# Performance work log

Hardware: AMD Instinct MI355X
Metric: run time of the kernel (lower is better)

Reference implementation:

```python
import jax, jax.numpy as jnp
import numpy as np

B, F, H, OUT, S = 32768, 256, 128, 64, 6
RELAX, EPS, BN_EPS = 1.5, 1e-05, 1e-05
SQRT_HALF = 0.7071067811865476


def _bn(h, g, b):
    # training-mode BatchNorm1d: biased batch statistics over dim 0
    m = h.mean(axis=0)
    v = h.var(axis=0)
    return (h - m) * jax.lax.rsqrt(v + BN_EPS) * g + b


def _tfrm(x, W, g, b, glu_act=True):
    h = _bn(x @ W, g, b)
    if glu_act:
        d = h.shape[1] // 2
        h = h[:, :d] * jax.nn.sigmoid(h[:, d:])
    return h


def setup_inputs() -> dict:
    key = jax.random.key(0)
    ks = jax.random.split(key, 6)
    f32 = jnp.float32
    return {
        "x": jax.random.normal(ks[0], (B, F), f32),
        "enc_g": jnp.ones((F,), f32), "enc_b": jnp.zeros((F,), f32),
        "W1": jax.random.normal(ks[1], (F, 2 * H), f32) * 0.05,
        "g1": jnp.ones((2 * H,), f32), "b1": jnp.zeros((2 * H,), f32),
        "W2": jax.random.normal(ks[2], (H, 2 * H), f32) * 0.05,
        "g2": jnp.ones((2 * H,), f32), "b2": jnp.zeros((2 * H,), f32),
        "W3": jax.random.normal(ks[3], (S, H, 2 * H), f32) * 0.05,
        "g3": jnp.ones((S, 2 * H), f32), "b3": jnp.zeros((S, 2 * H), f32),
        "W4": jax.random.normal(ks[4], (S, H, 2 * H), f32) * 0.05,
        "g4": jnp.ones((S, 2 * H), f32), "b4": jnp.zeros((S, 2 * H), f32),
        "Wc": jax.random.normal(ks[5], (S - 1, OUT, F), f32) * 0.05,
        "gc": jnp.ones((S - 1, F), f32), "bc": jnp.zeros((S - 1, F), f32),
    }


def reference(x, enc_g, enc_b, W1, g1, b1, W2, g2, b2, W3, g3, b3,
              W4, g4, b4, Wc, gc, bc):
    x = _bn(x, enc_g, enc_b)                      # [B, F]
    masked = x
    compl = jnp.ones((x.shape[0], F), x.dtype)    # complementary aggregated mask
    agg_out, agg_entropy = [], []
    for ni in range(S):
        h = _tfrm(masked, W1, g1, b1)                             # [B, H]
        h = (_tfrm(h, W2, g2, b2) + h) * SQRT_HALF
        h = (_tfrm(h, W3[ni], g3[ni], b3[ni]) + h) * SQRT_HALF
        h = (_tfrm(h, W4[ni], g4[ni], b4[ni]) + h) * SQRT_HALF
        if ni > 0:
            # NOTE: source uses x (not h) here -- replicated faithfully
            agg_out.append(jax.nn.relu(x[:, :OUT]))
        fc = h[:, OUT:]                                           # [B, OUT]
        if ni < S - 1:
            coef = _tfrm(fc, Wc[ni], gc[ni], bc[ni], glu_act=False)  # [B, F]
            mask_values = jax.nn.softmax(coef * compl, axis=1)
            compl = compl * (RELAX - mask_values)
            agg_entropy.append(
                jnp.mean(jnp.sum(-mask_values * jnp.log(mask_values + EPS), axis=1))
                / (S - 1))
            masked = mask_values * x
    out = jnp.sum(jnp.stack(agg_out, axis=0), axis=0)   # [B, OUT]
    entropy = jnp.sum(jnp.stack(agg_entropy))           # scalar
    return (out, entropy)
```

## Files before the change

### kernel.cpp

```cpp
#include <hip/hip_runtime.h>
#include <math.h>

#define BSZ   32768
#define FDIM  256
#define HDIM  128
#define OUTD  64
#define SQRT_HALF 0.70710678118654752f
#define BN_EPS 1e-5f
#define SM_EPS 1e-5f
#define INV_B (1.0f / 32768.0f)
#define NCPY  8
#define SLOT  (NCPY * 512)
#define GRID  1024

#define SWZ(r, cb) ((((r) << 9) + (cb)) ^ (((r) & 7) << 4))

typedef __attribute__((ext_vector_type(8))) short bf16x8;
typedef __attribute__((ext_vector_type(4))) short bf16x4;
typedef __attribute__((ext_vector_type(4))) float f32x4;

__device__ __forceinline__ float b2f(unsigned short u) {
    return __uint_as_float(((unsigned int)u) << 16);
}
__device__ __forceinline__ unsigned short f2b(float f) {
    unsigned int u = __float_as_uint(f);
    u += 0x7fff + ((u >> 16) & 1);
    return (unsigned short)(u >> 16);
}

__device__ __forceinline__ void async16(const void* g, void* l) {
    __builtin_amdgcn_global_load_lds(
        (const __attribute__((address_space(1))) void*)(uintptr_t)g,
        (__attribute__((address_space(3))) void*)(unsigned int)(uintptr_t)l,
        16, 0, 0);
}

__device__ inline float waveMaxAll(float v) {
#pragma unroll
    for (int m = 32; m > 0; m >>= 1) v = fmaxf(v, __shfl_xor(v, m, 64));
    return v;
}
__device__ inline float waveSumAll(float v) {
#pragma unroll
    for (int m = 32; m > 0; m >>= 1) v += __shfl_xor(v, m, 64);
    return v;
}

__device__ __forceinline__ void grid_sync_sw(unsigned int* bar, unsigned int nb) {
    __syncthreads();
    if (threadIdx.x == 0) {
        __threadfence();
        unsigned int gen = __hip_atomic_load(bar + 1, __ATOMIC_RELAXED, __HIP_MEMORY_SCOPE_AGENT);
        unsigned int arr = __hip_atomic_fetch_add(bar, 1u, __ATOMIC_ACQ_REL, __HIP_MEMORY_SCOPE_AGENT);
        if (arr == nb - 1) {
            __hip_atomic_store(bar, 0u, __ATOMIC_RELAXED, __HIP_MEMORY_SCOPE_AGENT);
            __hip_atomic_fetch_add(bar + 1, 1u, __ATOMIC_RELEASE, __HIP_MEMORY_SCOPE_AGENT);
        } else {
            long spin = 0;
            while (__hip_atomic_load(bar + 1, __ATOMIC_ACQUIRE, __HIP_MEMORY_SCOPE_AGENT) == gen) {
                if (++spin > (1L << 24)) break;
                __builtin_amdgcn_s_sleep(2);
            }
        }
        __threadfence();
    }
    __syncthreads();
}

__device__ __forceinline__ void stage_B(short* Bs, const unsigned short* __restrict__ Wt,
                                        int K, int k0, int wave, int lane) {
    const int sr = lane >> 2;
    const int sc = (lane & 3) * 8;
#pragma unroll
    for (int t = 0; t < 4; ++t) {
        const int wr = wave * 64 + t * 16 + sr;
        async16(Wt + (size_t)wr * K + k0 + sc, (void*)(Bs + (wave * 4 + t) * 512 + lane * 8));
    }
}

__device__ __forceinline__ void gemm_core(const short* buf, short* Bs,
                                          const unsigned short* __restrict__ Wt, int K,
                                          int wave, int lane, f32x4 (&acc)[2][4]) {
    const int fm = lane & 15;
    const int fq = (lane >> 4) * 8;
#pragma unroll
    for (int i = 0; i < 2; ++i)
#pragma unroll
        for (int j = 0; j < 4; ++j)
            acc[i][j] = (f32x4){0.f, 0.f, 0.f, 0.f};

    for (int k0 = 0; k0 < K; k0 += 32) {
        __syncthreads();
        bf16x8 af[2], bfr[4];
#pragma unroll
        for (int i = 0; i < 2; ++i)
            af[i] = *(const bf16x8*)((const char*)buf + SWZ(i * 16 + fm, (k0 + fq) * 2));
#pragma unroll
        for (int j = 0; j < 4; ++j)
            bfr[j] = *(const bf16x8*)(Bs + (wave * 64 + j * 16 + fm) * 32 + fq);
#pragma unroll
        for (int i = 0; i < 2; ++i)
#pragma unroll
            for (int j = 0; j < 4; ++j)
                acc[i][j] = __builtin_amdgcn_mfma_f32_16x16x32_bf16(af[i], bfr[j], acc[i][j], 0, 0, 0);
        __syncthreads();
        if (k0 + 32 < K) stage_B(Bs, Wt, K, k0 + 32, wave, lane);
    }
}

__device__ __forceinline__ void stage_epilogue(f32x4 (&acc)[2][4], short* buf,
                                               float* redS, float* redQ,
                                               float* __restrict__ statsOut,
                                               int wave, int lane, int tid, int bcp) {
    const int fm = lane & 15;
    const int row4 = (lane >> 4) * 4;
    const int ocol = wave * 64 + fm;
#pragma unroll
    for (int i = 0; i < 2; ++i)
#pragma unroll
        for (int j = 0; j < 4; ++j)
#pragma unroll
            for (int r = 0; r < 4; ++r)
                *(short*)((char*)buf + SWZ(row4 + i * 16 + r, (ocol + j * 16) * 2)) =
                    (short)f2b(acc[i][j][r]);

#pragma unroll
    for (int j = 0; j < 4; ++j) {
        float s = 0.f, q = 0.f;
#pragma unroll
        for (int i = 0; i < 2; ++i)
#pragma unroll
            for (int r = 0; r < 4; ++r) {
                float v = acc[i][j][r];
                s += v; q += v * v;
            }
        s += __shfl_xor(s, 16, 64); s += __shfl_xor(s, 32, 64);
        q += __shfl_xor(q, 16, 64); q += __shfl_xor(q, 32, 64);
        if (lane < 16) {
            redS[wave * 64 + j * 16 + lane] = s;
            redQ[wave * 64 + j * 16 + lane] = q;
        }
    }
    __syncthreads();
    atomicAdd(&statsOut[bcp + tid], redS[tid]);
    atomicAdd(&statsOut[bcp + 256 + tid], redQ[tid]);
}

__device__ __forceinline__ void build_tbl_glu(const float* __restrict__ st,
                                              const float* __restrict__ pg,
                                              const float* __restrict__ pb,
                                              int colOff, int K, int tid, float* tbl) {
    if (tid < K) {
        const int ch = colOff + tid;
        const int cg = ch + 128;
        float sA = 0.f, qA = 0.f, sG = 0.f, qG = 0.f;
#pragma unroll
        for (int cp = 0; cp < NCPY; ++cp) {
            const float* p = st + cp * 512;
            sA += p[ch]; qA += p[256 + ch];
            sG += p[cg]; qG += p[256 + cg];
        }
        float ma = sA * INV_B, va = qA * INV_B - ma * ma;
        float scA = pg[ch] * rsqrtf(va + BN_EPS);
        tbl[tid] = scA; tbl[K + tid] = pb[ch] - ma * scA;
        float mg = sG * INV_B, vg = qG * INV_B - mg * mg;
        float scG = pg[cg] * rsqrtf(vg + BN_EPS);
        tbl[2 * K + tid] = scG; tbl[3 * K + tid] = pb[cg] - mg * scG;
    }
    __syncthreads();
}

__device__ __forceinline__ void build_tbl_mask(const float* __restrict__ st,
                                               const float* __restrict__ gcp,
                                               const float* __restrict__ bcp_,
                                               int tid, float* tbl) {
    float s = 0.f, q = 0.f;
#pragma unroll
    for (int cp = 0; cp < NCPY; ++cp) {
        s += st[cp * 512 + tid];
        q += st[cp * 512 + 256 + tid];
    }
    float mean = s * INV_B, var = q * INV_B - mean * mean;
    float scl = gcp[tid] * rsqrtf(var + BN_EPS);
    tbl[tid] = scl;
    tbl[256 + tid] = bcp_[tid] - mean * scl;
    __syncthreads();
}

template <int K, bool RES, bool WH, int RB>
__device__ __forceinline__ void glu_prologue(short* buf, const float* tbl,
                                             int tid, int colOff, bf16x4* h) {
    const int ar = tid >> 3;
    const int ac = (tid & 7) * 4;
#pragma unroll
    for (int c = 0; c < K / 32; ++c) {
        const int kk = c * 32 + ac;
        bf16x4 lo = *(const bf16x4*)((const char*)buf + SWZ(ar, (colOff + kk) * 2));
        bf16x4 hi = *(const bf16x4*)((const char*)buf + SWZ(ar, (colOff + kk + 128) * 2));
        float4 a0 = *(const float4*)&tbl[kk];
        float4 h0 = *(const float4*)&tbl[K + kk];
        float4 g0 = *(const float4*)&tbl[2 * K + kk];
        float4 s0 = *(const float4*)&tbl[3 * K + kk];
        const float scA[4] = {a0.x, a0.y, a0.z, a0.w};
        const float shA[4] = {h0.x, h0.y, h0.z, h0.w};
        const float scG[4] = {g0.x, g0.y, g0.z, g0.w};
        const float shG[4] = {s0.x, s0.y, s0.z, s0.w};
        bf16x4 o4;
#pragma unroll
        for (int e = 0; e < 4; ++e) {
            float na = b2f((unsigned short)lo[e]) * scA[e] + shA[e];
            float ng = b2f((unsigned short)hi[e]) * scG[e] + shG[e];
            float v = na * (1.0f / (1.0f + __expf(-ng)));
            if (RES) v = (v + b2f((unsigned short)h[RB + c][e])) * SQRT_HALF;
            o4[e] = (short)f2b(v);
        }
        *(bf16x4*)((char*)buf + SWZ(ar, kk * 2)) = o4;
        if (WH) h[c] = o4;
    }
}

template <int MODE>
__device__ __forceinline__ void mask_phase(short* buf, const float* tbl,
                                           const unsigned short* __restrict__ xb,
                                           unsigned short* cmpl, float* ent, float* went,
                                           int tid, int wave, int lane, int row0, int bid) {
    const int r = tid >> 3;
    const int cq = tid & 7;
    const size_t grow = (size_t)(row0 + r) * 256;

    float l[32];
    float mx = -1e30f;
#pragma unroll
    for (int e = 0; e < 4; ++e) {
        const int c = cq * 32 + e * 8;
        bf16x8 pv = *(const bf16x8*)((const char*)buf + SWZ(r, c * 2));
        bf16x8 cv;
        if (MODE != 0) cv = *(const bf16x8*)(cmpl + grow + c);
        float4 s0 = *(const float4*)&tbl[c], s1 = *(const float4*)&tbl[c + 4];
        float4 h0 = *(const float4*)&tbl[256 + c], h1 = *(const float4*)&tbl[256 + c + 4];
        const float* sp0 = (const float*)&s0; const float* sp1 = (const float*)&s1;
        const float* hp0 = (const float*)&h0; const float* hp1 = (const float*)&h1;
#pragma unroll
        for (int t = 0; t < 8; ++t) {
            float scl = (t < 4) ? sp0[t] : sp1[t - 4];
            float shf = (t < 4) ? hp0[t] : hp1[t - 4];
            float cl = (MODE != 0) ? b2f((unsigned short)cv[t]) : 1.0f;
            float v = (b2f((unsigned short)pv[t]) * scl + shf) * cl;
            l[e * 8 + t] = v;
            mx = fmaxf(mx, v);
        }
    }
    mx = fmaxf(mx, __shfl_xor(mx, 1, 64));
    mx = fmaxf(mx, __shfl_xor(mx, 2, 64));
    mx = fmaxf(mx, __shfl_xor(mx, 4, 64));

    float ssum = 0.f;
#pragma unroll
    for (int i = 0; i < 32; ++i) { l[i] = __expf(l[i] - mx); ssum += l[i]; }
    ssum += __shfl_xor(ssum, 1, 64);
    ssum += __shfl_xor(ssum, 2, 64);
    ssum += __shfl_xor(ssum, 4, 64);
    const float inv = 1.0f / ssum;

    float et = 0.f;
#pragma unroll
    for (int e = 0; e < 4; ++e) {
        const int c = cq * 32 + e * 8;
        bf16x8 xv, cv2;
        if (MODE != 2) xv = *(const bf16x8*)(xb + grow + c);
        if (MODE == 1) cv2 = *(const bf16x8*)(cmpl + grow + c);
        bf16x8 mo, co;
#pragma unroll
        for (int t = 0; t < 8; ++t) {
            float m = l[e * 8 + t] * inv;
            et -= m * __logf(m + SM_EPS);
            if (MODE != 2) {
                float cl = (MODE == 1) ? b2f((unsigned short)cv2[t]) : 1.0f;
                co[t] = (short)f2b(cl * (1.5f - m));
                mo[t] = (short)f2b(m * b2f((unsigned short)xv[t]));
            }
        }
        if (MODE != 2) {
            *(bf16x8*)(cmpl + grow + c) = co;
            *(bf16x8*)((char*)buf + SWZ(r, c * 2)) = mo;
        }
    }
    et += __shfl_xor(et, 1, 64);
    et += __shfl_xor(et, 2, 64);
    et += __shfl_xor(et, 4, 64);
    float wet = waveSumAll(et) * 0.125f;
    if (lane == 0) went[wave] = wet;
    __syncthreads();
    if (tid == 0) {
        float v = went[0] + went[1] + went[2] + went[3];
        atomicAdd(&ent[(bid & 255) << 5], v * (INV_B * 0.2f));
    }
}

__global__ __launch_bounds__(256, 4) void mega(
    const float* __restrict__ x,
    const float* __restrict__ enc_g, const float* __restrict__ enc_b,
    const float* __restrict__ g1, const float* __restrict__ b1,
    const float* __restrict__ g2, const float* __restrict__ b2,
    const float* __restrict__ g3, const float* __restrict__ b3,
    const float* __restrict__ g4, const float* __restrict__ b4,
    const float* __restrict__ gc, const float* __restrict__ bc,
    const float* __restrict__ W1f, const float* __restrict__ W2f,
    const float* __restrict__ W3f, const float* __restrict__ W4f,
    const float* __restrict__ Wcf,
    unsigned short* __restrict__ W1t, unsigned short* __restrict__ W2t,
    unsigned short* __restrict__ W3t, unsigned short* __restrict__ W4t,
    unsigned short* __restrict__ Wct,
    unsigned short* __restrict__ xb, unsigned short* __restrict__ cmpl,
    float* __restrict__ stats, float* __restrict__ ent,
    unsigned int* __restrict__ bar,
    float* __restrict__ out)
{
#define GSYNC() grid_sync_sw(bar, GRID)

    __shared__ short buf[32 * 256];
    __shared__ short Bs[256 * 32];
    __shared__ float redS[256], redQ[256];
    __shared__ float tbl[512];
    __shared__ float went[4];

    const int tid  = threadIdx.x;
    const int wave = tid >> 6;
    const int lane = tid & 63;
    const int bid  = blockIdx.x;
    const int row0 = bid * 32;
    const int bcp  = (bid & (NCPY - 1)) * 512;

    if (bid < 136) {
        const int m = bid >> 3, kz = bid & 7, n = tid;
        const float* src; unsigned short* dst; int K;
        if (m == 0)      { src = W1f;                        dst = W1t;               K = 256; }
        else if (m == 1) { src = W2f;                        dst = W2t;               K = 128; }
        else if (m < 7)  { int i = m - 2;  src = W3f + (size_t)i * 128 * 256; dst = W3t + (size_t)i * 32768; K = 128; }
        else if (m < 12) { int i = m - 7;  src = W4f + (size_t)i * 128 * 256; dst = W4t + (size_t)i * 32768; K = 128; }
        else             { int i = m - 12; src = Wcf + (size_t)i * 64 * 256;  dst = Wct + (size_t)i * 16384; K = 64; }
        const int k0 = kz * 32;
        if (k0 < K)
            for (int k = k0; k < k0 + 32; ++k)
                dst[(size_t)n * K + k] = f2b(src[(size_t)k * 256 + n]);
    }
    {
        float* red = (float*)buf;
        const int sub = wave;
        const int c4  = lane << 2;
        float s[4] = {0.f, 0.f, 0.f, 0.f}, q[4] = {0.f, 0.f, 0.f, 0.f};
#pragma unroll 8
        for (int i = 0; i < 8; ++i) {
            const int row = row0 + i * 4 + sub;
            float4 v = *(const float4*)(x + (size_t)row * 256 + c4);
            s[0] += v.x; q[0] += v.x * v.x;
            s[1] += v.y; q[1] += v.y * v.y;
            s[2] += v.z; q[2] += v.z * v.z;
            s[3] += v.w; q[3] += v.w * v.w;
        }
#pragma unroll
        for (int e = 0; e < 4; ++e) {
            red[sub * 512 + c4 + e] = s[e];
            red[sub * 512 + 256 + c4 + e] = q[e];
        }
        __syncthreads();
        float sS = red[tid] + red[512 + tid] + red[1024 + tid] + red[1536 + tid];
        float sQ = red[256 + tid] + red[768 + tid] + red[1280 + tid] + red[1792 + tid];
        atomicAdd(&stats[bcp + tid], sS);
        atomicAdd(&stats[bcp + 256 + tid], sQ);
    }
    GSYNC();

    stage_B(Bs, W1t, 256, 0, wave, lane);
    {
        float s = 0.f, q = 0.f;
#pragma unroll
        for (int cp = 0; cp < NCPY; ++cp) {
            s += stats[cp * 512 + tid];
            q += stats[cp * 512 + 256 + tid];
        }
        float mean = s * INV_B, var = q * INV_B - mean * mean;
        float scl = enc_g[tid] * rsqrtf(var + BN_EPS);
        tbl[tid] = scl;
        tbl[256 + tid] = enc_b[tid] - mean * scl;
    }
    __syncthreads();
    {
        const int r = tid >> 3, cq = tid & 7;
        const size_t grow = (size_t)(row0 + r) * 256;
#pragma unroll
        for (int e = 0; e < 4; ++e) {
            const int c = cq * 32 + e * 8;
            float4 xa = *(const float4*)(x + grow + c);
            float4 xc = *(const float4*)(x + grow + c + 4);
            const float xv[8] = {xa.x, xa.y, xa.z, xa.w, xc.x, xc.y, xc.z, xc.w};
            float4 s0 = *(const float4*)&tbl[c], s1 = *(const float4*)&tbl[c + 4];
            float4 f0 = *(const float4*)&tbl[256 + c], f1 = *(const float4*)&tbl[256 + c + 4];
            const float sc[8] = {s0.x, s0.y, s0.z, s0.w, s1.x, s1.y, s1.z, s1.w};
            const float sh[8] = {f0.x, f0.y, f0.z, f0.w, f1.x, f1.y, f1.z, f1.w};
            float n[8];
            bf16x8 o8;
#pragma unroll
            for (int t = 0; t < 8; ++t) {
                n[t] = xv[t] * sc[t] + sh[t];
                o8[t] = (short)f2b(n[t]);
            }
            *(bf16x8*)((char*)buf + SWZ(r, c * 2)) = o8;
            *(bf16x8*)(xb + grow + c) = o8;
            if (c < OUTD) {
                float4 o1 = make_float4(5.f * fmaxf(n[0], 0.f), 5.f * fmaxf(n[1], 0.f),
                                        5.f * fmaxf(n[2], 0.f), 5.f * fmaxf(n[3], 0.f));
                float4 o2 = make_float4(5.f * fmaxf(n[4], 0.f), 5.f * fmaxf(n[5], 0.f),
                                        5.f * fmaxf(n[6], 0.f), 5.f * fmaxf(n[7], 0.f));
                *(float4*)(out + (size_t)(row0 + r) * OUTD + c) = o1;
                *(float4*)(out + (size_t)(row0 + r) * OUTD + c + 4) = o2;
            }
        }
    }

    f32x4 acc[2][4];
    bf16x4 h[4];

    for (int ni = 0; ni < 5; ++ni) {
        float* s1 = stats + (size_t)(1 + ni * 5 + 0) * SLOT;
        float* s2 = stats + (size_t)(1 + ni * 5 + 1) * SLOT;
        float* s3 = stats + (size_t)(1 + ni * 5 + 2) * SLOT;
        float* s4 = stats + (size_t)(1 + ni * 5 + 3) * SLOT;
        float* s5 = stats + (size_t)(1 + ni * 5 + 4) * SLOT;

        if (ni > 0) {
            stage_B(Bs, W1t, 256, 0, wave, lane);
            float* s5p = stats + (size_t)(1 + (ni - 1) * 5 + 4) * SLOT;
            build_tbl_mask(s5p, gc + (ni - 1) * 256, bc + (ni - 1) * 256, tid, tbl);
            if (ni == 1)
                mask_phase<0>(buf, tbl, xb, cmpl, ent, went, tid, wave, lane, row0, bid);
            else
                mask_phase<1>(buf, tbl, xb, cmpl, ent, went, tid, wave, lane, row0, bid);
        }
        gemm_core(buf, Bs, W1t, 256, wave, lane, acc);
        stage_epilogue(acc, buf, redS, redQ, s1, wave, lane, tid, bcp);
        GSYNC();

        stage_B(Bs, W2t, 128, 0, wave, lane);
        build_tbl_glu(s1, g1, b1, 0, 128, tid, tbl);
        glu_prologue<128, false, true, 0>(buf, tbl, tid, 0, h);
        gemm_core(buf, Bs, W2t, 128, wave, lane, acc);
        stage_epilogue(acc, buf, redS, redQ, s2, wave, lane, tid, bcp);
        GSYNC();

        {
            const unsigned short* Wt = W3t + (size_t)ni * 32768;
            stage_B(Bs, Wt, 128, 0, wave, lane);
            build_tbl_glu(s2, g2, b2, 0, 128, tid, tbl);
            glu_prologue<128, true, true, 0>(buf, tbl, tid, 0, h);
            gemm_core(buf, Bs, Wt, 128, wave, lane, acc);
            stage_epilogue(acc, buf, redS, redQ, s3, wave, lane, tid, bcp);
        }
        GSYNC();

        {
            const unsigned short* Wt = W4t + (size_t)ni * 32768;
            stage_B(Bs, Wt, 128, 0, wave, lane);
            build_tbl_glu(s3, g3 + ni * 256, b3 + ni * 256, 0, 128, tid, tbl);
            glu_prologue<128, true, true, 0>(buf, tbl, tid, 0, h);
            gemm_core(buf, Bs, Wt, 128, wave, lane, acc);
            stage_epilogue(acc, buf, redS, redQ, s4, wave, lane, tid, bcp);
        }
        GSYNC();

        {
            const unsigned short* Wt = Wct + (size_t)ni * 16384;
            stage_B(Bs, Wt, 64, 0, wave, lane);
            build_tbl_glu(s4, g4 + ni * 256, b4 + ni * 256, 64, 64, tid, tbl);
            glu_prologue<64, true, false, 2>(buf, tbl, tid, 64, h);
            gemm_core(buf, Bs, Wt, 64, wave, lane, acc);
            stage_epilogue(acc, buf, redS, redQ, s5, wave, lane, tid, bcp);
        }
        GSYNC();
    }

    build_tbl_mask(stats + (size_t)(1 + 4 * 5 + 4) * SLOT,
                   gc + 4 * 256, bc + 4 * 256, tid, tbl);
    mask_phase<2>(buf, tbl, xb, cmpl, ent, went, tid, wave, lane, row0, bid);
    GSYNC();

    if (bid == 0 && wave == 0) {
        float v = 0.f;
#pragma unroll
        for (int i = 0; i < 4; ++i) v += ent[(lane + 64 * i) << 5];
        v = waveSumAll(v);
        if (lane == 0) out[(size_t)BSZ * OUTD] = v;
    }
#undef GSYNC
}

__global__ __launch_bounds__(256) void prep_w(
    const float* __restrict__ W1, const float* __restrict__ W2,
    const float* __restrict__ W3, const float* __restrict__ W4,
    const float* __restrict__ Wc,
    unsigned short* __restrict__ W1t, unsigned short* __restrict__ W2t,
    unsigned short* __restrict__ W3t, unsigned short* __restrict__ W4t,
    unsigned short* __restrict__ Wct)
{
    const int m = blockIdx.x, kz = blockIdx.y, n = threadIdx.x;
    const float* src; unsigned short* dst; int K;
    if (m == 0)      { src = W1;                        dst = W1t;               K = 256; }
    else if (m == 1) { src = W2;                        dst = W2t;               K = 128; }
    else if (m < 7)  { int i = m - 2;  src = W3 + (size_t)i * 128 * 256; dst = W3t + (size_t)i * 32768; K = 128; }
    else if (m < 12) { int i = m - 7;  src = W4 + (size_t)i * 128 * 256; dst = W4t + (size_t)i * 32768; K = 128; }
    else             { int i = m - 12; src = Wc + (size_t)i * 64 * 256;  dst = Wct + (size_t)i * 16384; K = 64; }
    const int k0 = kz * 32;
    if (k0 >= K) return;
    for (int k = k0; k < k0 + 32; ++k)
        dst[(size_t)n * K + k] = f2b(src[(size_t)k * 256 + n]);
}

__global__ __launch_bounds__(256) void colstats(const float* __restrict__ X,
                                                float* __restrict__ st0) {
    __shared__ float red[4][512];
    const int sub = threadIdx.x >> 6;
    const int c4  = (threadIdx.x & 63) << 2;
    float s[4] = {0.f, 0.f, 0.f, 0.f}, q[4] = {0.f, 0.f, 0.f, 0.f};
#pragma unroll 8
    for (int i = 0; i < 8; ++i) {
        const int row = blockIdx.x * 32 + i * 4 + sub;
        float4 v = *(const float4*)(X + (size_t)row * 256 + c4);
        s[0] += v.x; q[0] += v.x * v.x;
        s[1] += v.y; q[1] += v.y * v.y;
        s[2] += v.z; q[2] += v.z * v.z;
        s[3] += v.w; q[3] += v.w * v.w;
    }
#pragma unroll
    for (int e = 0; e < 4; ++e) {
        red[sub][c4 + e] = s[e];
        red[sub][256 + c4 + e] = q[e];
    }
    __syncthreads();
    const int t = threadIdx.x;
    const int cp = (blockIdx.x & (NCPY - 1)) * 512;
    float sS = red[0][t] + red[1][t] + red[2][t] + red[3][t];
    float sQ = red[0][256 + t] + red[1][256 + t] + red[2][256 + t] + red[3][256 + t];
    atomicAdd(&st0[cp + t], sS);
    atomicAdd(&st0[cp + 256 + t], sQ);
}

__global__ __launch_bounds__(256) void norm_x(const float* __restrict__ x,
                                              const float* __restrict__ st0,
                                              const float* __restrict__ g,
                                              const float* __restrict__ b,
                                              unsigned short* __restrict__ xb,
                                              float* __restrict__ out) {
    const int i4 = blockIdx.x * 256 + threadIdx.x;
    const int row = i4 >> 6, c4 = (i4 & 63) << 2;
    float4 xv = *(const float4*)(x + (size_t)row * 256 + c4);
    float sS[4] = {0.f, 0.f, 0.f, 0.f}, sQ[4] = {0.f, 0.f, 0.f, 0.f};
#pragma unroll
    for (int cp = 0; cp < NCPY; ++cp) {
        float4 a = *(const float4*)&st0[cp * 512 + c4];
        float4 q = *(const float4*)&st0[cp * 512 + 256 + c4];
        sS[0] += a.x; sS[1] += a.y; sS[2] += a.z; sS[3] += a.w;
        sQ[0] += q.x; sQ[1] += q.y; sQ[2] += q.z; sQ[3] += q.w;
    }
    float4 gv = *(const float4*)&g[c4];
    float4 bv = *(const float4*)&b[c4];
    const float* xp = (const float*)&xv;
    const float* gp = (const float*)&gv; const float* bp = (const float*)&bv;
    float n[4];
    ushort4 ob;
    unsigned short* obp = (unsigned short*)&ob;
#pragma unroll
    for (int e = 0; e < 4; ++e) {
        float mean = sS[e] * INV_B;
        float var  = sQ[e] * INV_B - mean * mean;
        float sc   = gp[e] * rsqrtf(var + BN_EPS);
        float sh   = bp[e] - mean * sc;
        n[e] = xp[e] * sc + sh;
        obp[e] = f2b(n[e]);
    }
    *(ushort4*)(xb + (size_t)row * 256 + c4) = ob;
    if (c4 < OUTD) {
        float4 ov = make_float4(5.0f * fmaxf(n[0], 0.f), 5.0f * fmaxf(n[1], 0.f),
                                5.0f * fmaxf(n[2], 0.f), 5.0f * fmaxf(n[3], 0.f));
        *(float4*)(out + (size_t)row * OUTD + c4) = ov;
    }
}

__device__ __forceinline__ void gemm_epilogue(
    f32x4 (&acc)[2][4], int row0, int wave, int lane, int tid, int bcp,
    float* redS, float* redQ,
    unsigned short* __restrict__ Pout, float* __restrict__ statsOut)
{
    const int fm = lane & 15;
    const int orow = row0 + (lane >> 4) * 4;
    const int ocol = wave * 64 + fm;
#pragma unroll
    for (int i = 0; i < 2; ++i)
#pragma unroll
        for (int j = 0; j < 4; ++j)
#pragma unroll
            for (int r = 0; r < 4; ++r)
                Pout[(size_t)(orow + i * 16 + r) * 256 + (ocol + j * 16)] = f2b(acc[i][j][r]);

#pragma unroll
    for (int j = 0; j < 4; ++j) {
        float s = 0.f, q = 0.f;
#pragma unroll
        for (int i = 0; i < 2; ++i)
#pragma unroll
            for (int r = 0; r < 4; ++r) {
                float v = acc[i][j][r];
                s += v; q += v * v;
            }
        s += __shfl_xor(s, 16, 64); s += __shfl_xor(s, 32, 64);
        q += __shfl_xor(q, 16, 64); q += __shfl_xor(q, 32, 64);
        if (lane < 16) {
            redS[wave * 64 + j * 16 + lane] = s;
            redQ[wave * 64 + j * 16 + lane] = q;
        }
    }
    __syncthreads();
    atomicAdd(&statsOut[bcp + tid], redS[tid]);
    atomicAdd(&statsOut[bcp + 256 + tid], redQ[tid]);
}

__global__ __launch_bounds__(256) void gemm_bf16(
    const unsigned short* __restrict__ A,
    const unsigned short* __restrict__ Wt, int K,
    unsigned short* __restrict__ P,
    float* __restrict__ statsOut)
{
    __shared__ short As[32 * 32];
    __shared__ short Bs[256 * 32];
    __shared__ float redS[256], redQ[256];

    const int tid  = threadIdx.x;
    const int wave = tid >> 6;
    const int lane = tid & 63;
    const int row0 = blockIdx.x * 32;
    const int bcp  = (blockIdx.x & (NCPY - 1)) * 512;

    const int sr = lane >> 2;
    const int sc = (lane & 3) * 8;
    const int fm = lane & 15;
    const int fq = (lane >> 4) * 8;

    f32x4 acc[2][4];
#pragma unroll
    for (int i = 0; i < 2; ++i)
#pragma unroll
        for (int j = 0; j < 4; ++j)
            acc[i][j] = (f32x4){0.f, 0.f, 0.f, 0.f};

    for (int k0 = 0; k0 < K; k0 += 32) {
        if (wave < 2)
            async16(A + (size_t)(row0 + wave * 16 + sr) * K + k0 + sc,
                    (void*)(As + wave * 512 + lane * 8));
#pragma unroll
        for (int t = 0; t < 4; ++t) {
            const int wr = wave * 64 + t * 16 + sr;
            async16(Wt + (size_t)wr * K + k0 + sc,
                    (void*)(Bs + (wave * 4 + t) * 512 + lane * 8));
        }
        __syncthreads();

        bf16x8 af[2], bfr[4];
#pragma unroll
        for (int i = 0; i < 2; ++i)
            af[i] = *(const bf16x8*)(As + (i * 16 + fm) * 32 + fq);
#pragma unroll
        for (int j = 0; j < 4; ++j)
            bfr[j] = *(const bf16x8*)(Bs + (wave * 64 + j * 16 + fm) * 32 + fq);
#pragma unroll
        for (int i = 0; i < 2; ++i)
#pragma unroll
            for (int j = 0; j < 4; ++j)
                acc[i][j] = __builtin_amdgcn_mfma_f32_16x16x32_bf16(af[i], bfr[j], acc[i][j], 0, 0, 0);
        __syncthreads();
    }

    gemm_epilogue(acc, row0, wave, lane, tid, bcp, redS, redQ, P, statsOut);
}

template <int MODE>
__global__ __launch_bounds__(256) void gemm_mask(
    const unsigned short* Pc,
    const float* __restrict__ cstats,
    const float* __restrict__ gc, const float* __restrict__ bc,
    const unsigned short* __restrict__ xb,
    unsigned short* __restrict__ cmpl,
    float* __restrict__ ent,
    const unsigned short* __restrict__ Wt,
    unsigned short* Pout,
    float* __restrict__ statsOut)
{
    __shared__ short Am[32 * 256];
    __shared__ short Bs[256 * 32];
    __shared__ float redS[256], redQ[256];
    __shared__ float tScl[256], tShf[256];
    __shared__ float went[4];

    const int tid  = threadIdx.x;
    const int wave = tid >> 6;
    const int lane = tid & 63;
    const int row0 = blockIdx.x * 32;
    const int bcp  = (blockIdx.x & (NCPY - 1)) * 512;

    const int sr = lane >> 2;
    const int sc = (lane & 3) * 8;

#pragma unroll
    for (int t = 0; t < 4; ++t) {
        const int wr = wave * 64 + t * 16 + sr;
        async16(Wt + (size_t)wr * 256 + sc,
                (void*)(Bs + (wave * 4 + t) * 512 + lane * 8));
    }

    {
        float s = 0.f, q = 0.f;
#pragma unroll
        for (int cp = 0; cp < NCPY; ++cp) {
            s += cstats[cp * 512 + tid];
            q += cstats[cp * 512 + 256 + tid];
        }
        float mean = s * INV_B, var = q * INV_B - mean * mean;
        float scl_ = gc[tid] * rsqrtf(var + BN_EPS);
        tScl[tid] = scl_;
        tShf[tid] = bc[tid] - mean * scl_;
    }
    __syncthreads();

    const int r  = tid >> 3;
    const int cq = tid & 7;
    const size_t grow = (size_t)(row0 + r) * 256;

    float l[32];
    float mx = -1e30f;
#pragma unroll
    for (int e = 0; e < 4; ++e) {
        const int c = cq * 32 + e * 8;
        bf16x8 pv = *(const bf16x8*)(Pc + grow + c);
        bf16x8 cv;
        if (MODE) cv = *(const bf16x8*)(cmpl + grow + c);
        float4 s0 = *(const float4*)&tScl[c], s1 = *(const float4*)&tScl[c + 4];
        float4 h0 = *(const float4*)&tShf[c], h1 = *(const float4*)&tShf[c + 4];
        const float* sp0 = (const float*)&s0; const float* sp1 = (const float*)&s1;
        const float* hp0 = (const float*)&h0; const float* hp1 = (const float*)&h1;
#pragma unroll
        for (int t = 0; t < 8; ++t) {
            float scl_ = (t < 4) ? sp0[t] : sp1[t - 4];
            float shf_ = (t < 4) ? hp0[t] : hp1[t - 4];
            float cl = MODE ? b2f((unsigned short)cv[t]) : 1.0f;
            float v = (b2f((unsigned short)pv[t]) * scl_ + shf_) * cl;
            l[e * 8 + t] = v;
            mx = fmaxf(mx, v);
        }
    }
    mx = fmaxf(mx, __shfl_xor(mx, 1, 64));
    mx = fmaxf(mx, __shfl_xor(mx, 2, 64));
    mx = fmaxf(mx, __shfl_xor(mx, 4, 64));

    float ssum = 0.f;
#pragma unroll
    for (int i = 0; i < 32; ++i) { l[i] = __expf(l[i] - mx); ssum += l[i]; }
    ssum += __shfl_xor(ssum, 1, 64);
    ssum += __shfl_xor(ssum, 2, 64);
    ssum += __shfl_xor(ssum, 4, 64);
    const float inv = 1.0f / ssum;

    float et = 0.f;
#pragma unroll
    for (int e = 0; e < 4; ++e) {
        const int c = cq * 32 + e * 8;
        bf16x8 xv = *(const bf16x8*)(xb + grow + c);
        bf16x8 cv2;
        if (MODE) cv2 = *(const bf16x8*)(cmpl + grow + c);
        bf16x8 mo, co;
#pragma unroll
        for (int t = 0; t < 8; ++t) {
            float m = l[e * 8 + t] * inv;
            et -= m * __logf(m + SM_EPS);
            float cl = MODE ? b2f((unsigned short)cv2[t]) : 1.0f;
            co[t] = (short)f2b(cl * (1.5f - m));
            mo[t] = (short)f2b(m * b2f((unsigned short)xv[t]));
        }
        *(bf16x8*)(cmpl + grow + c) = co;
        unsigned int byte = (unsigned int)(r * 512 + c * 2);
        byte ^= ((unsigned int)(r & 7)) << 4;
        *(bf16x8*)((char*)Am + byte) = mo;
    }
    et += __shfl_xor(et, 1, 64);
    et += __shfl_xor(et, 2, 64);
    et += __shfl_xor(et, 4, 64);
    float wet = waveSumAll(et) * 0.125f;
    if (lane == 0) went[wave] = wet;
    __syncthreads();
    if (tid == 0) {
        float v = went[0] + went[1] + went[2] + went[3];
        atomicAdd(&ent[(blockIdx.x & 255) << 5], v * (INV_B * 0.2f));
    }

    const int fm = lane & 15;
    const int fq = (lane >> 4) * 8;

    f32x4 acc[2][4];
#pragma unroll
    for (int i = 0; i < 2; ++i)
#pragma unroll
        for (int j = 0; j < 4; ++j)
            acc[i][j] = (f32x4){0.f, 0.f, 0.f, 0.f};

    for (int k0 = 0; k0 < 256; k0 += 32) {
        bf16x8 af[2], bfr[4];
#pragma unroll
        for (int i = 0; i < 2; ++i) {
            const int row = i * 16 + fm;
            unsigned int byte = (unsigned int)(row * 512 + (k0 + fq) * 2);
            byte ^= ((unsigned int)(row & 7)) << 4;
            af[i] = *(const bf16x8*)((const char*)Am + byte);
        }
#pragma unroll
        for (int j = 0; j < 4; ++j)
            bfr[j] = *(const bf16x8*)(Bs + (wave * 64 + j * 16 + fm) * 32 + fq);
#pragma unroll
        for (int i = 0; i < 2; ++i)
#pragma unroll
            for (int j = 0; j < 4; ++j)
                acc[i][j] = __builtin_amdgcn_mfma_f32_16x16x32_bf16(af[i], bfr[j], acc[i][j], 0, 0, 0);
        __syncthreads();
        if (k0 + 32 < 256) {
#pragma unroll
            for (int t = 0; t < 4; ++t) {
                const int wr = wave * 64 + t * 16 + sr;
                async16(Wt + (size_t)wr * 256 + (k0 + 32) + sc,
                        (void*)(Bs + (wave * 4 + t) * 512 + lane * 8));
            }
            __syncthreads();
        }
    }

    gemm_epilogue(acc, row0, wave, lane, tid, bcp, redS, redQ, Pout, statsOut);
}

template <bool RES, bool WRITE_H>
__global__ __launch_bounds__(256) void gemm_glu(
    const unsigned short* __restrict__ Pprev,
    const float* __restrict__ pstats,
    const float* __restrict__ pg,
    const float* __restrict__ pb,
    const unsigned short* __restrict__ res,
    int colOff,
    const unsigned short* __restrict__ Wt, int K,
    unsigned short* __restrict__ Pout,
    float* __restrict__ statsOut,
    unsigned short* __restrict__ hOut)
{
    __shared__ short As[32 * 32];
    __shared__ short Bs[256 * 32];
    __shared__ float redS[256], redQ[256];
    __shared__ float tScA[128], tShA[128], tScG[128], tShG[128];

    const int tid  = threadIdx.x;
    const int wave = tid >> 6;
    const int lane = tid & 63;
    const int row0 = blockIdx.x * 32;
    const int bcp  = (blockIdx.x & (NCPY - 1)) * 512;

    if (tid < K) {
        const int ch = colOff + tid;
        const int cg = ch + 128;
        float sA = 0.f, qA = 0.f, sG = 0.f, qG = 0.f;
#pragma unroll
        for (int cp = 0; cp < NCPY; ++cp) {
            const float* p = pstats + cp * 512;
            sA += p[ch]; qA += p[256 + ch];
            sG += p[cg]; qG += p[256 + cg];
        }
        float ma = sA * INV_B, va = qA * INV_B - ma * ma;
        float scA = pg[ch] * rsqrtf(va + BN_EPS);
        tScA[tid] = scA; tShA[tid] = pb[ch] - ma * scA;
        float mg = sG * INV_B, vg = qG * INV_B - mg * mg;
        float scG = pg[cg] * rsqrtf(vg + BN_EPS);
        tScG[tid] = scG; tShG[tid] = pb[cg] - mg * scG;
    }
    __syncthreads();

    const int sr = lane >> 2;
    const int sc = (lane & 3) * 8;
    const int ar = tid >> 3;
    const int ac = (tid & 7) * 4;
    const int fm = lane & 15;
    const int fq = (lane >> 4) * 8;

    f32x4 acc[2][4];
#pragma unroll
    for (int i = 0; i < 2; ++i)
#pragma unroll
        for (int j = 0; j < 4; ++j)
            acc[i][j] = (f32x4){0.f, 0.f, 0.f, 0.f};

    for (int k0 = 0; k0 < K; k0 += 32) {
#pragma unroll
        for (int t = 0; t < 4; ++t) {
            const int wr = wave * 64 + t * 16 + sr;
            async16(Wt + (size_t)wr * K + k0 + sc,
                    (void*)(Bs + (wave * 4 + t) * 512 + lane * 8));
        }

        {
            const int kk = k0 + ac;
            const size_t grow = (size_t)(row0 + ar);

            bf16x4 lo = *(const bf16x4*)(Pprev + grow * 256 + colOff + kk);
            bf16x4 hi = *(const bf16x4*)(Pprev + grow * 256 + colOff + kk + 128);
            bf16x4 rv;
            if (RES) rv = *(const bf16x4*)(res + grow * 128 + kk);

            float4 a0 = *(const float4*)&tScA[kk];
            float4 h0 = *(const float4*)&tShA[kk];
            float4 g0 = *(const float4*)&tScG[kk];
            float4 s0 = *(const float4*)&tShG[kk];
            float scA[4] = {a0.x, a0.y, a0.z, a0.w};
            float shA[4] = {h0.x, h0.y, h0.z, h0.w};
            float scG[4] = {g0.x, g0.y, g0.z, g0.w};
            float shG[4] = {s0.x, s0.y, s0.z, s0.w};

            bf16x4 o4;
#pragma unroll
            for (int e = 0; e < 4; ++e) {
                float na = b2f((unsigned short)lo[e]) * scA[e] + shA[e];
                float ng = b2f((unsigned short)hi[e]) * scG[e] + shG[e];
                float v = na * (1.0f / (1.0f + __expf(-ng)));
                if (RES) v = (v + b2f((unsigned short)rv[e])) * SQRT_HALF;
                o4[e] = (short)f2b(v);
            }
            *(bf16x4*)(As + ar * 32 + ac) = o4;
            if (WRITE_H)
                *(bf16x4*)(hOut + grow * 128 + kk) = o4;
        }
        __syncthreads();

        bf16x8 af[2], bfr[4];
#pragma unroll
        for (int i = 0; i < 2; ++i)
            af[i] = *(const bf16x8*)(As + (i * 16 + fm) * 32 + fq);
#pragma unroll
        for (int j = 0; j < 4; ++j)
            bfr[j] = *(const bf16x8*)(Bs + (wave * 64 + j * 16 + fm) * 32 + fq);
#pragma unroll
        for (int i = 0; i < 2; ++i)
#pragma unroll
            for (int j = 0; j < 4; ++j)
                acc[i][j] = __builtin_amdgcn_mfma_f32_16x16x32_bf16(af[i], bfr[j], acc[i][j], 0, 0, 0);
        __syncthreads();
    }

    gemm_epilogue(acc, row0, wave, lane, tid, bcp, redS, redQ, Pout, statsOut);
}

__global__ __launch_bounds__(256) void coef_ent(const unsigned short* __restrict__ Pc,
                                                const float* __restrict__ stats,
                                                const float* __restrict__ gc,
                                                const float* __restrict__ bc,
                                                const unsigned short* __restrict__ cmpl,
                                                float* __restrict__ ent) {
    const int w    = threadIdx.x >> 6;
    const int lane = threadIdx.x & 63;
    const int row  = blockIdx.x * 4 + w;
    const int c    = lane << 2;
    __shared__ float went[4];

    float sS[4] = {0.f, 0.f, 0.f, 0.f}, sQ[4] = {0.f, 0.f, 0.f, 0.f};
#pragma unroll
    for (int cp = 0; cp < NCPY; ++cp) {
        float4 a = *(const float4*)&stats[cp * 512 + c];
        float4 q = *(const float4*)&stats[cp * 512 + 256 + c];
        sS[0] += a.x; sS[1] += a.y; sS[2] += a.z; sS[3] += a.w;
        sQ[0] += q.x; sQ[1] += q.y; sQ[2] += q.z; sQ[3] += q.w;
    }
    float4 gv = *(const float4*)&gc[c];
    float4 bv = *(const float4*)&bc[c];
    const float* gvv = (const float*)&gv; const float* bvv = (const float*)&bv;

    float scl[4], shf[4];
#pragma unroll
    for (int e = 0; e < 4; ++e) {
        float mean = sS[e] * INV_B, var = sQ[e] * INV_B - mean * mean;
        scl[e] = gvv[e] * rsqrtf(var + BN_EPS);
        shf[e] = bvv[e] - mean * scl[e];
    }

    const size_t idx = (size_t)row * 256 + c;
    ushort4 pu = *(const ushort4*)(Pc + idx);
    const unsigned short* puv = (const unsigned short*)&pu;
    ushort4 cu = *(const ushort4*)(cmpl + idx);
    const unsigned short* cuv = (const unsigned short*)&cu;

    float l[4];
#pragma unroll
    for (int e = 0; e < 4; ++e)
        l[e] = (b2f(puv[e]) * scl[e] + shf[e]) * b2f(cuv[e]);

    float mx = waveMaxAll(fmaxf(fmaxf(l[0], l[1]), fmaxf(l[2], l[3])));
    float e0 = __expf(l[0] - mx), e1 = __expf(l[1] - mx),
          e2 = __expf(l[2] - mx), e3 = __expf(l[3] - mx);
    float inv = 1.0f / waveSumAll(e0 + e1 + e2 + e3);

    float m[4] = {e0 * inv, e1 * inv, e2 * inv, e3 * inv};

    float et = -m[0] * __logf(m[0] + SM_EPS) - m[1] * __logf(m[1] + SM_EPS)
             - m[2] * __logf(m[2] + SM_EPS) - m[3] * __logf(m[3] + SM_EPS);
    et = waveSumAll(et);
    if (lane == 0) went[w] = et;
    __syncthreads();
    if (threadIdx.x == 0) {
        float v = went[0] + went[1] + went[2] + went[3];
        atomicAdd(&ent[(blockIdx.x & 255) << 5], v * (INV_B * 0.2f));
    }
}

__global__ __launch_bounds__(64) void write_ent(const float* __restrict__ ent,
                                                float* __restrict__ dst) {
    const int lane = threadIdx.x;
    float v = 0.f;
#pragma unroll
    for (int i = 0; i < 4; ++i) v += ent[(lane + 64 * i) << 5];
    v = waveSumAll(v);
    if (lane == 0) dst[0] = v;
}

extern "C" void kernel_launch(void* const* d_in, const int* in_sizes, int n_in,
                              void* d_out, int out_size, void* d_ws, size_t ws_size,
                              hipStream_t stream) {
    const float* x     = (const float*)d_in[0];
    const float* enc_g = (const float*)d_in[1];
    const float* enc_b = (const float*)d_in[2];
    const float* W1 = (const float*)d_in[3];
    const float* g1 = (const float*)d_in[4];
    const float* b1 = (const float*)d_in[5];
    const float* W2 = (const float*)d_in[6];
    const float* g2 = (const float*)d_in[7];
    const float* b2 = (const float*)d_in[8];
    const float* W3 = (const float*)d_in[9];
    const float* g3 = (const float*)d_in[10];
    const float* b3 = (const float*)d_in[11];
    const float* W4 = (const float*)d_in[12];
    const float* g4 = (const float*)d_in[13];
    const float* b4 = (const float*)d_in[14];
    const float* Wc = (const float*)d_in[15];
    const float* gc = (const float*)d_in[16];
    const float* bc = (const float*)d_in[17];
    float* out = (float*)d_out;

    const size_t NBF = (size_t)BSZ * FDIM;
    const size_t NBH = (size_t)BSZ * HDIM;

    unsigned short* xb     = (unsigned short*)d_ws;
    unsigned short* masked = xb + NBF;
    unsigned short* Pb1    = masked + NBF;
    unsigned short* h1     = Pb1 + NBF;
    unsigned short* h2     = h1 + NBH;
    unsigned short* h3     = h2 + NBH;
    unsigned short* cmpl   = h3 + NBH;
    unsigned short* W1t    = cmpl + NBF;
    unsigned short* W2t    = W1t + 65536;
    unsigned short* W3t    = W2t + 32768;
    unsigned short* W4t    = W3t + 163840;
    unsigned short* Wct    = W4t + 163840;
    float* stats = (float*)(Wct + 81920);
    float* ent   = stats + 26 * SLOT;
    unsigned int* bar = (unsigned int*)masked;

    unsigned short* Pb2 = masked;

    static int s_ok = -1;
    if (s_ok < 0) {
        int occ = 0, mpc = 0, dev = 0;
        hipGetDevice(&dev);
        hipDeviceProp_t prop;
        if (hipGetDeviceProperties(&prop, dev) == hipSuccess) mpc = prop.multiProcessorCount;
        if (hipOccupancyMaxActiveBlocksPerMultiprocessor(
                &occ, reinterpret_cast<const void*>(mega), 256, 0) != hipSuccess) occ = 0;
        s_ok = (occ >= 4 && occ * mpc >= GRID) ? 1 : 0;
    }

    hipMemsetAsync(stats, 0, (26 * SLOT + 256 * 32) * sizeof(float), stream);

    if (s_ok) {
        hipMemsetAsync(bar, 0, 2 * sizeof(unsigned int), stream);
        mega<<<GRID, 256, 0, stream>>>(
            x, enc_g, enc_b, g1, b1, g2, b2, g3, b3, g4, b4, gc, bc,
            W1, W2, W3, W4, Wc, W1t, W2t, W3t, W4t, Wct,
            xb, cmpl, stats, ent, bar, out);
        return;
    }

    prep_w<<<dim3(17, 8), 256, 0, stream>>>(W1, W2, W3, W4, Wc, W1t, W2t, W3t, W4t, Wct);
    colstats<<<1024, 256, 0, stream>>>(x, stats);
    norm_x<<<8192, 256, 0, stream>>>(x, stats, enc_g, enc_b, xb, out);

    for (int ni = 0; ni < 5; ++ni) {
        float* s1 = stats + (size_t)(1 + ni * 5 + 0) * SLOT;
        float* s2 = stats + (size_t)(1 + ni * 5 + 1) * SLOT;
        float* s3 = stats + (size_t)(1 + ni * 5 + 2) * SLOT;
        float* s4 = stats + (size_t)(1 + ni * 5 + 3) * SLOT;
        float* s5 = stats + (size_t)(1 + ni * 5 + 4) * SLOT;

        if (ni == 0) {
            gemm_bf16<<<1024, 256, 0, stream>>>(xb, W1t, 256, Pb1, s1);
        } else {
            float* s5p = stats + (size_t)(1 + (ni - 1) * 5 + 4) * SLOT;
            if (ni == 1)
                gemm_mask<0><<<1024, 256, 0, stream>>>(
                    Pb1, s5p, gc, bc, xb, cmpl, ent, W1t, Pb1, s1);
            else
                gemm_mask<1><<<1024, 256, 0, stream>>>(
                    Pb1, s5p, gc + (ni - 1) * 256, bc + (ni - 1) * 256,
                    xb, cmpl, ent, W1t, Pb1, s1);
        }

        gemm_glu<false, true><<<1024, 256, 0, stream>>>(
            Pb1, s1, g1, b1, nullptr, 0, W2t, 128, Pb2, s2, h1);
        gemm_glu<true, true><<<1024, 256, 0, stream>>>(
            Pb2, s2, g2, b2, h1, 0, W3t + (size_t)ni * 32768, 128, Pb1, s3, h2);
        gemm_glu<true, true><<<1024, 256, 0, stream>>>(
            Pb1, s3, g3 + ni * 256, b3 + ni * 256, h2, 0,
            W4t + (size_t)ni * 32768, 128, Pb2, s4, h3);
        gemm_glu<true, false><<<1024, 256, 0, stream>>>(
            Pb2, s4, g4 + ni * 256, b4 + ni * 256, h3 + 64, 64,
            Wct + (size_t)ni * 16384, 64, Pb1, s5, nullptr);
    }

    coef_ent<<<BSZ / 4, 256, 0, stream>>>(
        Pb1, stats + (size_t)(1 + 4 * 5 + 4) * SLOT,
        gc + 4 * 256, bc + 4 * 256, cmpl, ent);

    write_ent<<<1, 64, 0, stream>>>(ent, out + (size_t)BSZ * OUTD);
}
```

Measured before the change: 565.5 us.

## Replace central grid barrier with striped counters and prefetch next weights before sync

The single-counter generation barrier becomes 64 striped monotonic counters. Each block increments one counter and 64 threads poll all of them against a running target, which spreads atomic contention and removes the reset step. The first weight tile of the next stage is now issued asynchronously before the barrier, so its load overlaps the wait. This relies on the staged B tile not being overwritten by anything in between, and on the barrier memory being enlarged and zeroed each launch.

```diff
diff --git a/kernel.cpp b/kernel.cpp
--- a/kernel.cpp
+++ b/kernel.cpp
@@ -46,21 +46,20 @@
     return v;
 }
 
-__device__ __forceinline__ void grid_sync_sw(unsigned int* bar, unsigned int nb) {
-    __syncthreads();
-    if (threadIdx.x == 0) {
+__device__ __forceinline__ void grid_sync_tree(unsigned int* arr, unsigned int want,
+                                               int bid, int tid) {
+    __syncthreads();
+    if (tid == 0) {
         __threadfence();
-        unsigned int gen = __hip_atomic_load(bar + 1, __ATOMIC_RELAXED, __HIP_MEMORY_SCOPE_AGENT);
-        unsigned int arr = __hip_atomic_fetch_add(bar, 1u, __ATOMIC_ACQ_REL, __HIP_MEMORY_SCOPE_AGENT);
-        if (arr == nb - 1) {
-            __hip_atomic_store(bar, 0u, __ATOMIC_RELAXED, __HIP_MEMORY_SCOPE_AGENT);
-            __hip_atomic_fetch_add(bar + 1, 1u, __ATOMIC_RELEASE, __HIP_MEMORY_SCOPE_AGENT);
-        } else {
-            long spin = 0;
-            while (__hip_atomic_load(bar + 1, __ATOMIC_ACQUIRE, __HIP_MEMORY_SCOPE_AGENT) == gen) {
-                if (++spin > (1L << 24)) break;
-                __builtin_amdgcn_s_sleep(2);
-            }
+        __hip_atomic_fetch_add(&arr[(bid & 63) << 5], 1u,
+                               __ATOMIC_RELEASE, __HIP_MEMORY_SCOPE_AGENT);
+    }
+    if (tid < 64) {
+        unsigned int* p = &arr[tid << 5];
+        long spin = 0;
+        while (__hip_atomic_load(p, __ATOMIC_ACQUIRE, __HIP_MEMORY_SCOPE_AGENT) < want) {
+            if (++spin > (1L << 24)) break;
+            __builtin_amdgcn_s_sleep(1);
         }
         __threadfence();
     }
@@ -316,8 +315,6 @@
     unsigned int* __restrict__ bar,
     float* __restrict__ out)
 {
-#define GSYNC() grid_sync_sw(bar, GRID)
-
     __shared__ short buf[32 * 256];
     __shared__ short Bs[256 * 32];
     __shared__ float redS[256], redQ[256];
@@ -330,6 +327,9 @@
     const int bid  = blockIdx.x;
     const int row0 = bid * 32;
     const int bcp  = (bid & (NCPY - 1)) * 512;
+
+    unsigned int bgen = 0;
+#define GSYNC() do { ++bgen; grid_sync_tree(bar, bgen * 16u, bid, tid); } while (0)
 
     if (bid < 136) {
         const int m = bid >> 3, kz = bid & 7, n = tid;
@@ -429,7 +429,6 @@
         float* s5 = stats + (size_t)(1 + ni * 5 + 4) * SLOT;
 
         if (ni > 0) {
-            stage_B(Bs, W1t, 256, 0, wave, lane);
             float* s5p = stats + (size_t)(1 + (ni - 1) * 5 + 4) * SLOT;
             build_tbl_mask(s5p, gc + (ni - 1) * 256, bc + (ni - 1) * 256, tid, tbl);
             if (ni == 1)
@@ -439,43 +438,35 @@
         }
         gemm_core(buf, Bs, W1t, 256, wave, lane, acc);
         stage_epilogue(acc, buf, redS, redQ, s1, wave, lane, tid, bcp);
+        stage_B(Bs, W2t, 128, 0, wave, lane);
         GSYNC();
 
-        stage_B(Bs, W2t, 128, 0, wave, lane);
         build_tbl_glu(s1, g1, b1, 0, 128, tid, tbl);
         glu_prologue<128, false, true, 0>(buf, tbl, tid, 0, h);
         gemm_core(buf, Bs, W2t, 128, wave, lane, acc);
         stage_epilogue(acc, buf, redS, redQ, s2, wave, lane, tid, bcp);
+        stage_B(Bs, W3t + (size_t)ni * 32768, 128, 0, wave, lane);
         GSYNC();
 
-        {
-            const unsigned short* Wt = W3t + (size_t)ni * 32768;
-            stage_B(Bs, Wt, 128, 0, wave, lane);
-            build_tbl_glu(s2, g2, b2, 0, 128, tid, tbl);
-            glu_prologue<128, true, true, 0>(buf, tbl, tid, 0, h);
-            gemm_core(buf, Bs, Wt, 128, wave, lane, acc);
-            stage_epilogue(acc, buf, redS, redQ, s3, wave, lane, tid, bcp);
-        }
+        build_tbl_glu(s2, g2, b2, 0, 128, tid, tbl);
+        glu_prologue<128, true, true, 0>(buf, tbl, tid, 0, h);
+        gemm_core(buf, Bs, W3t + (size_t)ni * 32768, 128, wave, lane, acc);
+        stage_epilogue(acc, buf, redS, redQ, s3, wave, lane, tid, bcp);
+        stage_B(Bs, W4t + (size_t)ni * 32768, 128, 0, wave, lane);
         GSYNC();
 
-        {
-            const unsigned short* Wt = W4t + (size_t)ni * 32768;
-            stage_B(Bs, Wt, 128, 0, wave, lane);
-            build_tbl_glu(s3, g3 + ni * 256, b3 + ni * 256, 0, 128, tid, tbl);
-            glu_prologue<128, true, true, 0>(buf, tbl, tid, 0, h);
-            gemm_core(buf, Bs, Wt, 128, wave, lane, acc);
-            stage_epilogue(acc, buf, redS, redQ, s4, wave, lane, tid, bcp);
-        }
+        build_tbl_glu(s3, g3 + ni * 256, b3 + ni * 256, 0, 128, tid, tbl);
+        glu_prologue<128, true, true, 0>(buf, tbl, tid, 0, h);
+        gemm_core(buf, Bs, W4t + (size_t)ni * 32768, 128, wave, lane, acc);
+        stage_epilogue(acc, buf, redS, redQ, s4, wave, lane, tid, bcp);
+        stage_B(Bs, Wct + (size_t)ni * 16384, 64, 0, wave, lane);
         GSYNC();
 
-        {
-            const unsigned short* Wt = Wct + (size_t)ni * 16384;
-            stage_B(Bs, Wt, 64, 0, wave, lane);
-            build_tbl_glu(s4, g4 + ni * 256, b4 + ni * 256, 64, 64, tid, tbl);
-            glu_prologue<64, true, false, 2>(buf, tbl, tid, 64, h);
-            gemm_core(buf, Bs, Wt, 64, wave, lane, acc);
-            stage_epilogue(acc, buf, redS, redQ, s5, wave, lane, tid, bcp);
-        }
+        build_tbl_glu(s4, g4 + ni * 256, b4 + ni * 256, 64, 64, tid, tbl);
+        glu_prologue<64, true, false, 2>(buf, tbl, tid, 64, h);
+        gemm_core(buf, Bs, Wct + (size_t)ni * 16384, 64, wave, lane, acc);
+        stage_epilogue(acc, buf, redS, redQ, s5, wave, lane, tid, bcp);
+        if (ni < 4) stage_B(Bs, W1t, 256, 0, wave, lane);
         GSYNC();
     }
 
@@ -1086,7 +1077,7 @@
     hipMemsetAsync(stats, 0, (26 * SLOT + 256 * 32) * sizeof(float), stream);
 
     if (s_ok) {
-        hipMemsetAsync(bar, 0, 2 * sizeof(unsigned int), stream);
+        hipMemsetAsync(bar, 0, 64 * 32 * sizeof(unsigned int), stream);
         mega<<<GRID, 256, 0, stream>>>(
             x, enc_g, enc_b, g1, b1, g2, b2, g3, b3, g4, b4, gc, bc,
             W1, W2, W3, W4, Wc, W1t, W2t, W3t, W4t, Wct,
```

New measurement: 560.2 us. Within noise of the previous version (-0.9%).
